# Kernel tuning notes

Hardware: AMD Instinct MI355X
Metric: run time of the kernel (lower is better)

The kernel has to match this reference:

```python
import jax, jax.numpy as jnp
import numpy as np

NEG_SLOPE = 0.2


def _gat_layer(x, W, a_src, a_dst, b, src, dst, n_nodes, heads, dim):
    # x: [N, F_in]; W: [F_in, heads*dim]
    h = (x @ W).reshape(n_nodes, heads, dim)            # [N,H,D]
    e_src = (h * a_src).sum(-1)                          # [N,H]
    e_dst = (h * a_dst).sum(-1)                          # [N,H]
    e = jax.nn.leaky_relu(e_src[src] + e_dst[dst], NEG_SLOPE)  # [E,H]
    # edge softmax over incoming edges of each target node
    m = jax.ops.segment_max(e, dst, num_segments=n_nodes)      # [N,H]
    ex = jnp.exp(e - m[dst])
    denom = jax.ops.segment_sum(ex, dst, num_segments=n_nodes)  # [N,H]
    alpha = ex / denom[dst]                              # [E,H]
    out = jax.ops.segment_sum(h[src] * alpha[:, :, None], dst,
                              num_segments=n_nodes)      # [N,H,D]
    return out.reshape(n_nodes, heads * dim) + b


def setup_inputs() -> dict:
    key = jax.random.key(0)
    ks = jax.random.split(key, 10)
    N, E, F_in = 100000, 1600000, 300
    x = jax.random.normal(ks[0], (N, F_in), dtype=jnp.float32)
    edge_index = jax.random.randint(ks[1], (2, E), 0, N, dtype=jnp.int64)
    s = 0.1
    return {
        'x': x,
        'edge_index': edge_index,
        'W1': jax.random.normal(ks[2], (F_in, 64), jnp.float32) * s,
        'att_src1': jax.random.normal(ks[3], (8, 8), jnp.float32) * s,
        'att_dst1': jax.random.normal(ks[4], (8, 8), jnp.float32) * s,
        'b1': jax.random.normal(ks[5], (64,), jnp.float32) * s,
        'W2': jax.random.normal(ks[6], (64, 64), jnp.float32) * s,
        'att_src2': jax.random.normal(ks[7], (1, 64), jnp.float32) * s,
        'att_dst2': jax.random.normal(ks[8], (1, 64), jnp.float32) * s,
        'b2': jax.random.normal(ks[9], (64,), jnp.float32) * s,
    }


def reference(x, edge_index, W1, att_src1, att_dst1, b1, W2, att_src2, att_dst2, b2):
    N = x.shape[0]
    # add self-loops (PyG GATConv default)
    loop = jnp.arange(N, dtype=edge_index.dtype)
    src = jnp.concatenate([edge_index[0], loop])
    dst = jnp.concatenate([edge_index[1], loop])
    # dropout p=0.6 is identity in eval mode
    h = _gat_layer(x, W1, att_src1, att_dst1, b1, src, dst, N, 8, 8)    # [N,64]
    h = jax.nn.elu(h)
    h = _gat_layer(h, W2, att_src2, att_dst2, b2, src, dst, N, 1, 64)   # [N,64]
    return jax.nn.log_softmax(h, axis=1)
```

## Files before the change

kernel.cpp:

```cpp
#include <hip/hip_runtime.h>
#include <math.h>

using short8  = __attribute__((ext_vector_type(8))) short;
using ushort8 = __attribute__((ext_vector_type(8))) unsigned short;
using f32x4   = __attribute__((ext_vector_type(4))) float;

#define NBLKS 512
#define BPAD  800
#define EB 8
#define BSTR 328

__device__ __forceinline__ unsigned short f2bf(float f) {
    unsigned u = __float_as_uint(f);
    unsigned r = u + 0x7FFF + ((u >> 16) & 1);
    return (unsigned short)(r >> 16);
}
__device__ __forceinline__ float bf2f(unsigned short v) {
    return __uint_as_float((unsigned)v << 16);
}
__device__ __forceinline__ unsigned cvt2(float lo, float hi) {
    unsigned r;
    asm("v_cvt_pk_bf16_f32 %0, %1, %2" : "=v"(r) : "v"(lo), "v"(hi));
    return r;
}
__device__ __forceinline__ float4 loadA(const float* __restrict__ p, int k) {
    return (k + 4 <= 300) ? *(const float4*)(p + k) : make_float4(0.f, 0.f, 0.f, 0.f);
}


__global__ void detect64_kernel(const int* __restrict__ ei, int E, int* __restrict__ flag) {
    __shared__ int any;
    if (threadIdx.x == 0) any = 0;
    __syncthreads();
    for (int i = threadIdx.x; i < 1024; i += 256) {
        if (ei[2 * i + 1] != 0) { any = 1; break; }
    }
    __syncthreads();
    if (threadIdx.x == 0) *flag = (any ? 0 : 1);
}


__global__ __launch_bounds__(256) void binA_kernel(
    const int* __restrict__ ei, int E, int N, const int* __restrict__ flag,
    int nbuck, int* __restrict__ hist, int chunk) {
    __shared__ int lh[BPAD];
    for (int i = threadIdx.x; i < nbuck; i += 256) lh[i] = 0;
    __syncthreads();
    int is64 = *flag;
    int Etot = E + N;
    int beg = blockIdx.x * chunk, end = min(Etot, beg + chunk);
    for (int i = beg + threadIdx.x; i < end; i += 256) {
        int d = (i < E) ? (is64 ? ei[2 * (E + i)] : ei[E + i]) : (i - E);
        atomicAdd(&lh[d >> 7], 1);
    }
    __syncthreads();
    for (int i = threadIdx.x; i < nbuck; i += 256) hist[blockIdx.x * BPAD + i] = lh[i];
}

__global__ void scanBlocks_kernel(int* __restrict__ hist, int nbuck, int* __restrict__ bucketTotal) {
    int bin = blockIdx.x * 256 + threadIdx.x;
    if (bin >= nbuck) return;
    int run = 0;
    for (int b = 0; b < NBLKS; b++) {
        int v = hist[b * BPAD + bin];
        hist[b * BPAD + bin] = run;
        run += v;
    }
    bucketTotal[bin] = run;
}

__global__ void scanBucket_kernel(const int* __restrict__ bucketTotal, int nbuck,
                                  int* __restrict__ bucketBase) {
    __shared__ int s[1024];
    int t = threadIdx.x;
    int v = (t < nbuck) ? bucketTotal[t] : 0;
    s[t] = v;
    __syncthreads();
    for (int off = 1; off < 1024; off <<= 1) {
        int x = (t >= off) ? s[t - off] : 0;
        __syncthreads();
        s[t] += x;
        __syncthreads();
    }
    if (t < nbuck) bucketBase[t] = s[t] - v;
    if (t == nbuck - 1) bucketBase[nbuck] = s[t];
}

__global__ __launch_bounds__(256) void binB_kernel(
    const int* __restrict__ ei, int E, int N, const int* __restrict__ flag,
    int nbuck, const int* __restrict__ hist, const int* __restrict__ bucketBase,
    int* __restrict__ tmp, int chunk) {
    __shared__ int cur[BPAD];
    for (int i = threadIdx.x; i < nbuck; i += 256)
        cur[i] = bucketBase[i] + hist[blockIdx.x * BPAD + i];
    __syncthreads();
    int is64 = *flag;
    int Etot = E + N;
    int beg = blockIdx.x * chunk, end = min(Etot, beg + chunk);
    for (int i = beg + threadIdx.x; i < end; i += 256) {
        int s, d;
        if (i < E) {
            if (is64) { s = ei[2 * i]; d = ei[2 * (E + i)]; }
            else      { s = ei[i];     d = ei[E + i]; }
        } else { s = i - E; d = i - E; }
        int pos = atomicAdd(&cur[d >> 7], 1);
        tmp[pos] = ((d & 127) << 17) | s;
    }
}

__global__ __launch_bounds__(256) void binC_kernel(
    const int* __restrict__ tmp, const int* __restrict__ bucketBase, int nbuck,
    int N, int Etot, int* __restrict__ rowptr, int* __restrict__ col) {
    __shared__ int lh[128];
    __shared__ int cur[128];
    int g = blockIdx.x;
    int t = threadIdx.x;
    int beg = bucketBase[g], end = bucketBase[g + 1];
    if (t < 128) lh[t] = 0;
    __syncthreads();
    for (int i = beg + t; i < end; i += 256) atomicAdd(&lh[tmp[i] >> 17], 1);
    __syncthreads();
    int c = (t < 128) ? lh[t] : 0;
    for (int off = 1; off < 128; off <<= 1) {
        int x = 0;
        if (t < 128 && t >= off) x = lh[t - off];
        __syncthreads();
        if (t < 128) lh[t] += x;
        __syncthreads();
    }
    if (t < 128) {
        int excl = lh[t] - c;
        cur[t] = beg + excl;
        int node = g * 128 + t;
        if (node < N) rowptr[node] = beg + excl;
    }
    if (g == 0 && t == 0) rowptr[N] = Etot;
    if (g == 0 && t < 16) col[Etot + t] = 0;
    __syncthreads();
    for (int i = beg + t; i < end; i += 256) {
        int v = tmp[i];
        int pos = atomicAdd(&cur[v >> 17], 1);
        col[pos] = v & 0x1FFFF;
    }
}


__global__ __launch_bounds__(512) void gemm1_mfma_kernel(
    const float* __restrict__ x, const float* __restrict__ W,
    const float* __restrict__ asrc, const float* __restrict__ adst,
    unsigned short* __restrict__ hbf, float* __restrict__ es, float* __restrict__ ed, int N) {
    __shared__ __align__(16) unsigned short B_lds[64 * BSTR];
    const int tx = threadIdx.x;
    const int wv = tx >> 6;
    const int lane = tx & 63;
    const int l15 = lane & 15;
    const int quad = lane >> 4;
    const int rowBase = blockIdx.x * 128;

    {
        int colB = tx & 63;
        int kb0 = (tx >> 6) * 40;
#pragma unroll
        for (int j = 0; j < 40; j++) {
            int k = kb0 + j;
            float v = (k < 300) ? W[(size_t)k * 64 + colB] : 0.f;
            B_lds[colB * BSTR + k] = f2bf(v);
        }
    }
    __syncthreads();

    f32x4 acc[4];
#pragma unroll
    for (int ct = 0; ct < 4; ct++) acc[ct] = (f32x4){0.f, 0.f, 0.f, 0.f};

    const int myrow = rowBase + wv * 16 + l15;
    const float* xr = x + (size_t)min(myrow, N - 1) * 300;
    const int kb = quad * 8;

    float4 c0 = loadA(xr, kb);
    float4 c1 = loadA(xr, kb + 4);
#pragma unroll
    for (int k0 = 0; k0 < 320; k0 += 32) {
        float4 n0, n1;
        if (k0 < 288) {
            n0 = loadA(xr, k0 + 32 + kb);
            n1 = loadA(xr, k0 + 36 + kb);
        } else {
            n0 = make_float4(0.f, 0.f, 0.f, 0.f);
            n1 = make_float4(0.f, 0.f, 0.f, 0.f);
        }
        union { unsigned u[4]; short8 s; } cv;
        cv.u[0] = cvt2(c0.x, c0.y);
        cv.u[1] = cvt2(c0.z, c0.w);
        cv.u[2] = cvt2(c1.x, c1.y);
        cv.u[3] = cvt2(c1.z, c1.w);
#pragma unroll
        for (int ct = 0; ct < 4; ct++) {
            short8 bfr = *(const short8*)&B_lds[(ct * 16 + l15) * BSTR + k0 + kb];
            acc[ct] = __builtin_amdgcn_mfma_f32_16x16x32_bf16(cv.s, bfr, acc[ct], 0, 0, 0);
        }
        c0 = n0; c1 = n1;
    }

    float as_v[4], ad_v[4];
#pragma unroll
    for (int ct = 0; ct < 4; ct++) {
        as_v[ct] = asrc[ct * 16 + l15];
        ad_v[ct] = adst[ct * 16 + l15];
    }
#pragma unroll
    for (int reg = 0; reg < 4; reg++) {
        int row = rowBase + wv * 16 + quad * 4 + reg;
        bool ok = (row < N);
#pragma unroll
        for (int ct = 0; ct < 4; ct++) {
            float v = acc[ct][reg];
            if (ok) hbf[(size_t)row * 64 + ct * 16 + l15] = f2bf(v);
            float ps = v * as_v[ct];
            float pd = v * ad_v[ct];
            ps += __shfl_xor(ps, 1); ps += __shfl_xor(ps, 2); ps += __shfl_xor(ps, 4);
            pd += __shfl_xor(pd, 1); pd += __shfl_xor(pd, 2); pd += __shfl_xor(pd, 4);
            if ((lane & 7) == 0 && ok) {
                int head = 2 * ct + ((lane >> 3) & 1);
                es[row * 8 + head] = ps;
                ed[row * 8 + head] = pd;
            }
        }
    }
}


__global__ __launch_bounds__(256) void gemm2_mfma_kernel(
    const unsigned short* __restrict__ xin, const float* __restrict__ W,
    const float* __restrict__ asrc, const float* __restrict__ adst,
    unsigned short* __restrict__ hbf, float* __restrict__ es, float* __restrict__ ed, int N) {
    __shared__ __align__(16) unsigned short A_lds[128 * 72];
    __shared__ __align__(16) unsigned short B_lds[64 * 72];
    const int tx = threadIdx.x;
    const int wv = tx >> 6;
    const int lane = tx & 63;
    const int l15 = lane & 15;
    const int quad = lane >> 4;
    const int rowBase = blockIdx.x * 128;

    f32x4 acc[2][4];
#pragma unroll
    for (int rt = 0; rt < 2; rt++)
#pragma unroll
        for (int ct = 0; ct < 4; ct++) acc[rt][ct] = (f32x4){0.f, 0.f, 0.f, 0.f};

    {
        int colB = tx & 63;
        int kk = (tx >> 6) * 16;
#pragma unroll
        for (int j = 0; j < 16; j++)
            B_lds[colB * 72 + kk + j] = f2bf(W[(size_t)(kk + j) * 64 + colB]);
    }
    {
        int kq = tx & 7, r0 = tx >> 3;
        const ushort8 z = (ushort8){0, 0, 0, 0, 0, 0, 0, 0};
#pragma unroll
        for (int p = 0; p < 4; p++) {
            int row = p * 32 + r0;
            int grow = rowBase + row;
            ushort8 v = z;
            if (grow < N) v = *(const ushort8*)&xin[(size_t)grow * 64 + kq * 8];
            *(ushort8*)&A_lds[row * 72 + kq * 8] = v;
        }
    }
    __syncthreads();
#pragma unroll
    for (int c = 0; c < 2; c++) {
        short8 af[2], bfr[4];
#pragma unroll
        for (int rt = 0; rt < 2; rt++)
            af[rt] = *(const short8*)&A_lds[(wv * 32 + rt * 16 + l15) * 72 + quad * 8 + c * 32];
#pragma unroll
        for (int ct = 0; ct < 4; ct++)
            bfr[ct] = *(const short8*)&B_lds[(ct * 16 + l15) * 72 + quad * 8 + c * 32];
#pragma unroll
        for (int rt = 0; rt < 2; rt++)
#pragma unroll
            for (int ct = 0; ct < 4; ct++)
                acc[rt][ct] = __builtin_amdgcn_mfma_f32_16x16x32_bf16(af[rt], bfr[ct], acc[rt][ct], 0, 0, 0);
    }

    float as_v[4], ad_v[4];
#pragma unroll
    for (int ct = 0; ct < 4; ct++) {
        as_v[ct] = asrc[ct * 16 + l15];
        ad_v[ct] = adst[ct * 16 + l15];
    }
#pragma unroll
    for (int rt = 0; rt < 2; rt++) {
#pragma unroll
        for (int reg = 0; reg < 4; reg++) {
            int row = rowBase + wv * 32 + rt * 16 + quad * 4 + reg;
            bool ok = (row < N);
            float ps = 0.f, pd = 0.f;
#pragma unroll
            for (int ct = 0; ct < 4; ct++) {
                float v = acc[rt][ct][reg];
                if (ok) hbf[(size_t)row * 64 + ct * 16 + l15] = f2bf(v);
                ps = fmaf(v, as_v[ct], ps);
                pd = fmaf(v, ad_v[ct], pd);
            }
            ps += __shfl_xor(ps, 1); ps += __shfl_xor(ps, 2);
            ps += __shfl_xor(ps, 4); ps += __shfl_xor(ps, 8);
            pd += __shfl_xor(pd, 1); pd += __shfl_xor(pd, 2);
            pd += __shfl_xor(pd, 4); pd += __shfl_xor(pd, 8);
            if (l15 == 0 && ok) { es[row] = ps; ed[row] = pd; }
        }
    }
}


__global__ __launch_bounds__(256) void agg1f_kernel(
    const int* __restrict__ rowptr, const int* __restrict__ col,
    const unsigned short* __restrict__ hbf, const float* __restrict__ es,
    const float* __restrict__ ed, const float* __restrict__ b,
    unsigned int* __restrict__ outbf, int N) {
    int node = blockIdx.x * 4 + (threadIdx.x >> 6);
    int lane = threadIdx.x & 63;
    if (node >= N) return;
    int half = lane >> 5, fl = lane & 31;
    int f0 = fl * 2, hh = fl >> 2;
    int beg = rowptr[node], end = rowptr[node + 1];
    float edv = ed[node * 8 + hh];
    float acc0 = 0.f, acc1 = 0.f, lsum = 0.f;
    for (int i = beg; i < end; i += 16) {
        int ei_[EB], ss[EB];
        float ev[EB];
        unsigned hp[EB];
#pragma unroll
        for (int j = 0; j < EB; j++) ei_[j] = i + 2 * j + half;
#pragma unroll
        for (int j = 0; j < EB; j++) ss[j] = col[(ei_[j] < end) ? ei_[j] : beg];
#pragma unroll
        for (int j = 0; j < EB; j++) ev[j] = es[ss[j] * 8 + hh];
#pragma unroll
        for (int j = 0; j < EB; j++) hp[j] = *(const unsigned*)&hbf[(size_t)ss[j] * 64 + f0];
#pragma unroll
        for (int j = 0; j < EB; j++) {
            float e = ev[j] + edv;
            e = (e > 0.f) ? e : 0.2f * e;
            float wj = __expf(fminf(e, 30.f));
            wj = (ei_[j] < end) ? wj : 0.f;
            lsum += wj;
            float lo = __uint_as_float(hp[j] << 16);
            float hi = __uint_as_float(hp[j] & 0xFFFF0000u);
            acc0 = fmaf(wj, lo, acc0);
            acc1 = fmaf(wj, hi, acc1);
        }
    }
    acc0 += __shfl_xor(acc0, 32);
    acc1 += __shfl_xor(acc1, 32);
    lsum += __shfl_xor(lsum, 32);
    float rinv = 1.f / lsum;
    float o0 = acc0 * rinv + b[f0];
    float o1 = acc1 * rinv + b[f0 + 1];
    o0 = (o0 > 0.f) ? o0 : expm1f(o0);
    o1 = (o1 > 0.f) ? o1 : expm1f(o1);
    if (half == 0) {
        unsigned pk = (unsigned)f2bf(o0) | ((unsigned)f2bf(o1) << 16);
        outbf[((size_t)node * 64 + f0) >> 1] = pk;
    }
}

__global__ __launch_bounds__(256) void agg2f_kernel(
    const int* __restrict__ rowptr, const int* __restrict__ col,
    const unsigned short* __restrict__ hbf, const float* __restrict__ es,
    const float* __restrict__ ed, const float* __restrict__ b,
    float* __restrict__ out, int N) {
    int node = blockIdx.x * 4 + (threadIdx.x >> 6);
    int lane = threadIdx.x & 63;
    if (node >= N) return;
    int half = lane >> 5, fl = lane & 31;
    int f0 = fl * 2;
    int beg = rowptr[node], end = rowptr[node + 1];
    float edv = ed[node];
    float acc0 = 0.f, acc1 = 0.f, lsum = 0.f;
    for (int i = beg; i < end; i += 16) {
        int ei_[EB], ss[EB];
        float ev[EB];
        unsigned hp[EB];
#pragma unroll
        for (int j = 0; j < EB; j++) ei_[j] = i + 2 * j + half;
#pragma unroll
        for (int j = 0; j < EB; j++) ss[j] = col[(ei_[j] < end) ? ei_[j] : beg];
#pragma unroll
        for (int j = 0; j < EB; j++) ev[j] = es[ss[j]];
#pragma unroll
        for (int j = 0; j < EB; j++) hp[j] = *(const unsigned*)&hbf[(size_t)ss[j] * 64 + f0];
#pragma unroll
        for (int j = 0; j < EB; j++) {
            float e = ev[j] + edv;
            e = (e > 0.f) ? e : 0.2f * e;
            float wj = __expf(fminf(e, 30.f));
            wj = (ei_[j] < end) ? wj : 0.f;
            lsum += wj;
            float lo = __uint_as_float(hp[j] << 16);
            float hi = __uint_as_float(hp[j] & 0xFFFF0000u);
            acc0 = fmaf(wj, lo, acc0);
            acc1 = fmaf(wj, hi, acc1);
        }
    }
    acc0 += __shfl_xor(acc0, 32);
    acc1 += __shfl_xor(acc1, 32);
    lsum += __shfl_xor(lsum, 32);
    float rinv = 1.f / lsum;
    float o0 = acc0 * rinv + b[f0];
    float o1 = acc1 * rinv + b[f0 + 1];
    float M = fmaxf(o0, o1);
    M = fmaxf(M, __shfl_xor(M, 1));  M = fmaxf(M, __shfl_xor(M, 2));
    M = fmaxf(M, __shfl_xor(M, 4));  M = fmaxf(M, __shfl_xor(M, 8));
    M = fmaxf(M, __shfl_xor(M, 16));
    float se = __expf(o0 - M) + __expf(o1 - M);
    se += __shfl_xor(se, 1);  se += __shfl_xor(se, 2);
    se += __shfl_xor(se, 4);  se += __shfl_xor(se, 8);
    se += __shfl_xor(se, 16);
    float ls = logf(se);
    if (half == 0) {
        float2 r = make_float2(o0 - M - ls, o1 - M - ls);
        *(float2*)&out[(size_t)node * 64 + f0] = r;
    }
}


extern "C" void kernel_launch(void* const* d_in, const int* in_sizes, int n_in,
                              void* d_out, int out_size, void* d_ws, size_t ws_size,
                              hipStream_t stream) {
    const float* x   = (const float*)d_in[0];
    const int*   ei  = (const int*)d_in[1];
    const float* W1  = (const float*)d_in[2];
    const float* as1 = (const float*)d_in[3];
    const float* ad1 = (const float*)d_in[4];
    const float* b1  = (const float*)d_in[5];
    const float* W2  = (const float*)d_in[6];
    const float* as2 = (const float*)d_in[7];
    const float* ad2 = (const float*)d_in[8];
    const float* b2  = (const float*)d_in[9];
    const int N = in_sizes[0] / 300;
    const int E = in_sizes[1] / 2;
    const int Etot = E + N;
    const int nbuck = (N + 127) >> 7;
    (void)n_in; (void)out_size; (void)ws_size;

    char* w = (char*)d_ws;
    auto alloc = [&](size_t bytes) -> char* {
        char* p = w;
        w += (bytes + 255) & ~(size_t)255;
        return p;
    };
    int*   flag        = (int*)alloc(256);
    int*   hist        = (int*)alloc((size_t)NBLKS * BPAD * 4);
    int*   bucketTotal = (int*)alloc((size_t)(BPAD + 1) * 4);
    int*   bucketBase  = (int*)alloc((size_t)(BPAD + 1) * 4);
    int*   tmp         = (int*)alloc((size_t)(Etot + 16) * 4);
    int*   rowptr      = (int*)alloc((size_t)(N + 1) * 4);
    int*   col         = (int*)alloc((size_t)(Etot + 16) * 4);
    unsigned short* h1  = (unsigned short*)alloc((size_t)N * 64 * 2);
    unsigned short* h1p = (unsigned short*)alloc((size_t)N * 64 * 2);
    float* es1         = (float*)alloc((size_t)N * 8 * 4);
    float* ed1         = (float*)alloc((size_t)N * 8 * 4);
    float* es2         = (float*)alloc((size_t)N * 4);
    float* ed2         = (float*)alloc((size_t)N * 4);
    unsigned short* h2 = h1;

    detect64_kernel<<<1, 256, 0, stream>>>(ei, E, flag);

    int chunk = (Etot + NBLKS - 1) / NBLKS;
    binA_kernel<<<NBLKS, 256, 0, stream>>>(ei, E, N, flag, nbuck, hist, chunk);
    scanBlocks_kernel<<<(nbuck + 255) / 256, 256, 0, stream>>>(hist, nbuck, bucketTotal);
    scanBucket_kernel<<<1, 1024, 0, stream>>>(bucketTotal, nbuck, bucketBase);
    binB_kernel<<<NBLKS, 256, 0, stream>>>(ei, E, N, flag, nbuck, hist, bucketBase, tmp, chunk);
    binC_kernel<<<nbuck, 256, 0, stream>>>(tmp, bucketBase, nbuck, N, Etot, rowptr, col);

    gemm1_mfma_kernel<<<(N + 127) / 128, 512, 0, stream>>>(x, W1, as1, ad1, h1, es1, ed1, N);
    agg1f_kernel<<<(N + 3) / 4, 256, 0, stream>>>(rowptr, col, h1, es1, ed1, b1,
                                                  (unsigned int*)h1p, N);
    gemm2_mfma_kernel<<<(N + 127) / 128, 256, 0, stream>>>(h1p, W2, as2, ad2, h2, es2, ed2, N);
    agg2f_kernel<<<(N + 3) / 4, 256, 0, stream>>>(rowptr, col, h2, es2, ed2, b2, (float*)d_out, N);
}
```

Measured before the change: 469.0 us.

## Stage GEMM1 A tiles via double-buffered direct global-to-LDS loads

The layer-1 GEMM now stages 128x32 fp32 tiles of x into XOR-swizzled, double-buffered LDS using global_load_lds DMA, instead of each lane loading float4 values straight into registers. Each wave now computes 32 rows (two MFMA row tiles) that share the same B fragments, and the block shrinks from 512 to 256 threads. The W staging also packs two bf16 values per store. The aim is to coalesce the streaming read of the 120 MB x matrix and overlap the next tile's load with the MFMAs. The cost is a barrier per K step and more LDS per block. Out-of-range K slots load arbitrary x data, which relies on the zero-padded B rows to cancel it.

```diff
diff --git a/kernel.cpp b/kernel.cpp
--- a/kernel.cpp
+++ b/kernel.cpp
@@ -23,8 +23,10 @@
     asm("v_cvt_pk_bf16_f32 %0, %1, %2" : "=v"(r) : "v"(lo), "v"(hi));
     return r;
 }
-__device__ __forceinline__ float4 loadA(const float* __restrict__ p, int k) {
-    return (k + 4 <= 300) ? *(const float4*)(p + k) : make_float4(0.f, 0.f, 0.f, 0.f);
+__device__ __forceinline__ void glds16(const void* g, void* l) {
+    __builtin_amdgcn_global_load_lds(
+        (const __attribute__((address_space(1))) unsigned*)g,
+        (__attribute__((address_space(3))) unsigned*)l, 16, 0, 0);
 }
 
 
@@ -145,11 +147,12 @@
 }
 
 
-__global__ __launch_bounds__(512) void gemm1_mfma_kernel(
+__global__ __launch_bounds__(256) void gemm1_mfma_kernel(
     const float* __restrict__ x, const float* __restrict__ W,
     const float* __restrict__ asrc, const float* __restrict__ adst,
     unsigned short* __restrict__ hbf, float* __restrict__ es, float* __restrict__ ed, int N) {
     __shared__ __align__(16) unsigned short B_lds[64 * BSTR];
+    __shared__ __align__(16) float A_lds[2][128 * 32];
     const int tx = threadIdx.x;
     const int wv = tx >> 6;
     const int lane = tx & 63;
@@ -157,49 +160,67 @@
     const int quad = lane >> 4;
     const int rowBase = blockIdx.x * 128;
 
+    const int sRowL = lane >> 3;
+    const int sSlot = lane & 7;
+
+    auto stageA = [&](int buf, int k0) {
+#pragma unroll
+        for (int j = 0; j < 4; j++) {
+            int row   = wv * 32 + j * 8 + sRowL;
+            int grow  = min(rowBase + row, N - 1);
+            int gslot = sSlot ^ (row & 7);
+            int koff  = k0 + gslot * 4;
+            size_t srcOff = (koff + 4 <= 300) ? ((size_t)grow * 300 + koff) : 0;
+            glds16(x + srcOff, &A_lds[buf][(wv * 32 + j * 8) * 32]);
+        }
+    };
+
+    f32x4 acc[2][4];
+#pragma unroll
+    for (int rt = 0; rt < 2; rt++)
+#pragma unroll
+        for (int ct = 0; ct < 4; ct++) acc[rt][ct] = (f32x4){0.f, 0.f, 0.f, 0.f};
+
+    stageA(0, 0);
     {
         int colB = tx & 63;
-        int kb0 = (tx >> 6) * 40;
+        int g4 = tx >> 6;
 #pragma unroll
         for (int j = 0; j < 40; j++) {
-            int k = kb0 + j;
-            float v = (k < 300) ? W[(size_t)k * 64 + colB] : 0.f;
-            B_lds[colB * BSTR + k] = f2bf(v);
-        }
-    }
-    __syncthreads();
-
-    f32x4 acc[4];
-#pragma unroll
-    for (int ct = 0; ct < 4; ct++) acc[ct] = (f32x4){0.f, 0.f, 0.f, 0.f};
-
-    const int myrow = rowBase + wv * 16 + l15;
-    const float* xr = x + (size_t)min(myrow, N - 1) * 300;
-    const int kb = quad * 8;
-
-    float4 c0 = loadA(xr, kb);
-    float4 c1 = loadA(xr, kb + 4);
-#pragma unroll
-    for (int k0 = 0; k0 < 320; k0 += 32) {
-        float4 n0, n1;
-        if (k0 < 288) {
-            n0 = loadA(xr, k0 + 32 + kb);
-            n1 = loadA(xr, k0 + 36 + kb);
-        } else {
-            n0 = make_float4(0.f, 0.f, 0.f, 0.f);
-            n1 = make_float4(0.f, 0.f, 0.f, 0.f);
-        }
-        union { unsigned u[4]; short8 s; } cv;
-        cv.u[0] = cvt2(c0.x, c0.y);
-        cv.u[1] = cvt2(c0.z, c0.w);
-        cv.u[2] = cvt2(c1.x, c1.y);
-        cv.u[3] = cvt2(c1.z, c1.w);
+            int k = (g4 * 40 + j) * 2;
+            float v0 = (k < 300)     ? W[(size_t)k * 64 + colB]       : 0.f;
+            float v1 = (k + 1 < 300) ? W[(size_t)(k + 1) * 64 + colB] : 0.f;
+            *(unsigned*)&B_lds[colB * BSTR + k] = cvt2(v0, v1);
+        }
+    }
+    __syncthreads();
+
+    for (int t = 0; t < 10; t++) {
+        int cur = t & 1;
+        if (t < 9) stageA(cur ^ 1, (t + 1) * 32);
+        short8 af[2];
+#pragma unroll
+        for (int rt = 0; rt < 2; rt++) {
+            int row = wv * 32 + rt * 16 + l15;
+            const float* ab = &A_lds[cur][row * 32];
+            int m = row & 7;
+            f32x4 fa = *(const f32x4*)(ab + (((2 * quad)     ^ m) * 4));
+            f32x4 fb = *(const f32x4*)(ab + (((2 * quad + 1) ^ m) * 4));
+            union { unsigned u[4]; short8 s; } cv;
+            cv.u[0] = cvt2(fa[0], fa[1]);
+            cv.u[1] = cvt2(fa[2], fa[3]);
+            cv.u[2] = cvt2(fb[0], fb[1]);
+            cv.u[3] = cvt2(fb[2], fb[3]);
+            af[rt] = cv.s;
+        }
+        const int k0 = t * 32;
 #pragma unroll
         for (int ct = 0; ct < 4; ct++) {
-            short8 bfr = *(const short8*)&B_lds[(ct * 16 + l15) * BSTR + k0 + kb];
-            acc[ct] = __builtin_amdgcn_mfma_f32_16x16x32_bf16(cv.s, bfr, acc[ct], 0, 0, 0);
-        }
-        c0 = n0; c1 = n1;
+            short8 bfr = *(const short8*)&B_lds[(ct * 16 + l15) * BSTR + k0 + quad * 8];
+            acc[0][ct] = __builtin_amdgcn_mfma_f32_16x16x32_bf16(af[0], bfr, acc[0][ct], 0, 0, 0);
+            acc[1][ct] = __builtin_amdgcn_mfma_f32_16x16x32_bf16(af[1], bfr, acc[1][ct], 0, 0, 0);
+        }
+        __syncthreads();
     }
 
     float as_v[4], ad_v[4];
@@ -209,21 +230,24 @@
         ad_v[ct] = adst[ct * 16 + l15];
     }
 #pragma unroll
-    for (int reg = 0; reg < 4; reg++) {
-        int row = rowBase + wv * 16 + quad * 4 + reg;
-        bool ok = (row < N);
-#pragma unroll
-        for (int ct = 0; ct < 4; ct++) {
-            float v = acc[ct][reg];
-            if (ok) hbf[(size_t)row * 64 + ct * 16 + l15] = f2bf(v);
-            float ps = v * as_v[ct];
-            float pd = v * ad_v[ct];
-            ps += __shfl_xor(ps, 1); ps += __shfl_xor(ps, 2); ps += __shfl_xor(ps, 4);
-            pd += __shfl_xor(pd, 1); pd += __shfl_xor(pd, 2); pd += __shfl_xor(pd, 4);
-            if ((lane & 7) == 0 && ok) {
-                int head = 2 * ct + ((lane >> 3) & 1);
-                es[row * 8 + head] = ps;
-                ed[row * 8 + head] = pd;
+    for (int rt = 0; rt < 2; rt++) {
+#pragma unroll
+        for (int reg = 0; reg < 4; reg++) {
+            int row = rowBase + wv * 32 + rt * 16 + quad * 4 + reg;
+            bool ok = (row < N);
+#pragma unroll
+            for (int ct = 0; ct < 4; ct++) {
+                float v = acc[rt][ct][reg];
+                if (ok) hbf[(size_t)row * 64 + ct * 16 + l15] = f2bf(v);
+                float ps = v * as_v[ct];
+                float pd = v * ad_v[ct];
+                ps += __shfl_xor(ps, 1); ps += __shfl_xor(ps, 2); ps += __shfl_xor(ps, 4);
+                pd += __shfl_xor(pd, 1); pd += __shfl_xor(pd, 2); pd += __shfl_xor(pd, 4);
+                if ((lane & 7) == 0 && ok) {
+                    int head = 2 * ct + ((lane >> 3) & 1);
+                    es[row * 8 + head] = ps;
+                    ed[row * 8 + head] = pd;
+                }
             }
         }
     }
@@ -476,7 +500,7 @@
     binB_kernel<<<NBLKS, 256, 0, stream>>>(ei, E, N, flag, nbuck, hist, bucketBase, tmp, chunk);
     binC_kernel<<<nbuck, 256, 0, stream>>>(tmp, bucketBase, nbuck, N, Etot, rowptr, col);
 
-    gemm1_mfma_kernel<<<(N + 127) / 128, 512, 0, stream>>>(x, W1, as1, ad1, h1, es1, ed1, N);
+    gemm1_mfma_kernel<<<(N + 127) / 128, 256, 0, stream>>>(x, W1, as1, ad1, h1, es1, ed1, N);
     agg1f_kernel<<<(N + 3) / 4, 256, 0, stream>>>(rowptr, col, h1, es1, ed1, b1,
                                                   (unsigned int*)h1p, N);
     gemm2_mfma_kernel<<<(N + 127) / 128, 256, 0, stream>>>(h1p, W2, as2, ad2, h2, es2, ed2, N);
```

After: 469.6 us. No clear change (+0.1%).

## Stream x tiles into LDS via global_load_lds and pre-transpose W1 to bf16

Applied to the files above, without the earlier changes.

The first-layer GEMM now copies each block's contiguous x rows straight into LDS with coalesced 16-byte global_load_lds instructions, replacing strided per-lane float4 loads. W1 is transposed and converted to bf16 once by a new small kernel instead of per block, and the B fragments are read from global or L2 with one-step register prefetch. The block shrinks to 48 rows and 192 threads to fit the fp32 A tile in LDS. The tail k-chunk reads the neighbouring row's data, which relies on the zero-padded Wt columns to cancel. It also adds an extra kernel launch.

```diff
diff --git a/kernel.cpp b/kernel.cpp
--- a/kernel.cpp
+++ b/kernel.cpp
@@ -8,7 +8,6 @@
 #define NBLKS 512
 #define BPAD  800
 #define EB 8
-#define BSTR 328
 
 __device__ __forceinline__ unsigned short f2bf(float f) {
     unsigned u = __float_as_uint(f);
@@ -23,8 +22,10 @@
     asm("v_cvt_pk_bf16_f32 %0, %1, %2" : "=v"(r) : "v"(lo), "v"(hi));
     return r;
 }
-__device__ __forceinline__ float4 loadA(const float* __restrict__ p, int k) {
-    return (k + 4 <= 300) ? *(const float4*)(p + k) : make_float4(0.f, 0.f, 0.f, 0.f);
+__device__ __forceinline__ void glds16(const void* g, void* l) {
+    __builtin_amdgcn_global_load_lds(
+        (const __attribute__((address_space(1))) unsigned*)g,
+        (__attribute__((address_space(3))) unsigned*)l, 16, 0, 0);
 }
 
 
@@ -145,61 +146,80 @@
 }
 
 
-__global__ __launch_bounds__(512) void gemm1_mfma_kernel(
-    const float* __restrict__ x, const float* __restrict__ W,
+__global__ __launch_bounds__(256) void wt1_kernel(const float* __restrict__ W,
+                                                  unsigned short* __restrict__ Wt) {
+    int idx = blockIdx.x * 256 + threadIdx.x;
+    if (idx >= 64 * 320) return;
+    int c = idx / 320, k = idx - c * 320;
+    float v = (k < 300) ? W[(size_t)k * 64 + c] : 0.f;
+    Wt[idx] = f2bf(v);
+}
+
+
+#define G1_ROWS 48
+#define G1_BYTES (G1_ROWS * 1200)
+#define G1_INSTR ((G1_BYTES + 1023) / 1024)
+
+__global__ __launch_bounds__(192) void gemm1_mfma_kernel(
+    const float* __restrict__ x, const unsigned short* __restrict__ Wt,
     const float* __restrict__ asrc, const float* __restrict__ adst,
     unsigned short* __restrict__ hbf, float* __restrict__ es, float* __restrict__ ed, int N) {
-    __shared__ __align__(16) unsigned short B_lds[64 * BSTR];
+    __shared__ __align__(16) float A_lds[G1_INSTR * 256];
     const int tx = threadIdx.x;
     const int wv = tx >> 6;
     const int lane = tx & 63;
     const int l15 = lane & 15;
     const int quad = lane >> 4;
-    const int rowBase = blockIdx.x * 128;
+    const int rowBase = blockIdx.x * G1_ROWS;
 
     {
-        int colB = tx & 63;
-        int kb0 = (tx >> 6) * 40;
-#pragma unroll
-        for (int j = 0; j < 40; j++) {
-            int k = kb0 + j;
-            float v = (k < 300) ? W[(size_t)k * 64 + colB] : 0.f;
-            B_lds[colB * BSTR + k] = f2bf(v);
-        }
-    }
-    __syncthreads();
+        const size_t regionByte = (size_t)rowBase * 1200;
+        const size_t lastOK = (size_t)N * 1200 - 16;
+        const char* xb = (const char*)x;
+#pragma unroll
+        for (int j = 0; j < 19; j++) {
+            int i = wv + 3 * j;
+            size_t g = regionByte + (size_t)i * 1024 + (size_t)lane * 16;
+            if (g > lastOK) g = lastOK;
+            glds16(xb + g, (char*)A_lds + i * 1024);
+        }
+    }
+
+    const unsigned short* wtl = Wt + (size_t)l15 * 320 + quad * 8;
+    ushort8 bcur[4];
+#pragma unroll
+    for (int ct = 0; ct < 4; ct++) bcur[ct] = *(const ushort8*)(wtl + ct * 16 * 320);
 
     f32x4 acc[4];
 #pragma unroll
     for (int ct = 0; ct < 4; ct++) acc[ct] = (f32x4){0.f, 0.f, 0.f, 0.f};
 
-    const int myrow = rowBase + wv * 16 + l15;
-    const float* xr = x + (size_t)min(myrow, N - 1) * 300;
-    const int kb = quad * 8;
-
-    float4 c0 = loadA(xr, kb);
-    float4 c1 = loadA(xr, kb + 4);
-#pragma unroll
-    for (int k0 = 0; k0 < 320; k0 += 32) {
-        float4 n0, n1;
-        if (k0 < 288) {
-            n0 = loadA(xr, k0 + 32 + kb);
-            n1 = loadA(xr, k0 + 36 + kb);
-        } else {
-            n0 = make_float4(0.f, 0.f, 0.f, 0.f);
-            n1 = make_float4(0.f, 0.f, 0.f, 0.f);
-        }
+    __syncthreads();
+
+    const float* arow = &A_lds[(wv * 16 + l15) * 300 + quad * 8];
+#pragma unroll
+    for (int t = 0; t < 10; t++) {
+        ushort8 bnext[4];
+        if (t < 9) {
+#pragma unroll
+            for (int ct = 0; ct < 4; ct++)
+                bnext[ct] = *(const ushort8*)(wtl + ct * 16 * 320 + (t + 1) * 32);
+        }
+        f32x4 fa = *(const f32x4*)(arow + t * 32);
+        f32x4 fb = *(const f32x4*)(arow + t * 32 + 4);
         union { unsigned u[4]; short8 s; } cv;
-        cv.u[0] = cvt2(c0.x, c0.y);
-        cv.u[1] = cvt2(c0.z, c0.w);
-        cv.u[2] = cvt2(c1.x, c1.y);
-        cv.u[3] = cvt2(c1.z, c1.w);
+        cv.u[0] = cvt2(fa[0], fa[1]);
+        cv.u[1] = cvt2(fa[2], fa[3]);
+        cv.u[2] = cvt2(fb[0], fb[1]);
+        cv.u[3] = cvt2(fb[2], fb[3]);
 #pragma unroll
         for (int ct = 0; ct < 4; ct++) {
-            short8 bfr = *(const short8*)&B_lds[(ct * 16 + l15) * BSTR + k0 + kb];
+            short8 bfr;
+            __builtin_memcpy(&bfr, &bcur[ct], 16);
             acc[ct] = __builtin_amdgcn_mfma_f32_16x16x32_bf16(cv.s, bfr, acc[ct], 0, 0, 0);
         }
-        c0 = n0; c1 = n1;
+#pragma unroll
+        for (int ct = 0; ct < 4; ct++) bcur[ct] = bnext[ct];
     }
 
     float as_v[4], ad_v[4];
@@ -465,6 +485,7 @@
     float* ed1         = (float*)alloc((size_t)N * 8 * 4);
     float* es2         = (float*)alloc((size_t)N * 4);
     float* ed2         = (float*)alloc((size_t)N * 4);
+    unsigned short* Wt1 = (unsigned short*)alloc((size_t)64 * 320 * 2);
     unsigned short* h2 = h1;
 
     detect64_kernel<<<1, 256, 0, stream>>>(ei, E, flag);
@@ -476,7 +497,9 @@
     binB_kernel<<<NBLKS, 256, 0, stream>>>(ei, E, N, flag, nbuck, hist, bucketBase, tmp, chunk);
     binC_kernel<<<nbuck, 256, 0, stream>>>(tmp, bucketBase, nbuck, N, Etot, rowptr, col);
 
-    gemm1_mfma_kernel<<<(N + 127) / 128, 512, 0, stream>>>(x, W1, as1, ad1, h1, es1, ed1, N);
+    wt1_kernel<<<(64 * 320 + 255) / 256, 256, 0, stream>>>(W1, Wt1);
+    gemm1_mfma_kernel<<<(N + G1_ROWS - 1) / G1_ROWS, 192, 0, stream>>>(
+        x, Wt1, as1, ad1, h1, es1, ed1, N);
     agg1f_kernel<<<(N + 3) / 4, 256, 0, stream>>>(rowptr, col, h1, es1, ed1, b1,
                                                   (unsigned int*)h1p, N);
     gemm2_mfma_kernel<<<(N + 127) / 128, 256, 0, stream>>>(h1p, W2, as2, ad2, h2, es2, ed2, N);
```

Result: no change. 463.5 us (-1.2%).
